# Kernel tuning notes

Measured on AMD Instinct MI355X. Metric: run time of the kernel, lower is better.

The kernel has to match this reference:

```python
import jax, jax.numpy as jnp
import numpy as np

T, D_IN, D_OUT = 8192, 1024, 1024
TRACE, CONTEXT = 64, 16


def setup_inputs() -> dict:
    key = jax.random.key(0)
    ks = jax.random.split(key, 8)
    x = jax.random.normal(ks[0], (T, D_IN), jnp.float32)
    state_re = jnp.zeros((1, TRACE, CONTEXT), jnp.float32)
    state_im = jnp.zeros((1, TRACE, CONTEXT), jnp.float32)
    start = jax.random.bernoulli(ks[1], 0.01, (T,))
    next_done = jax.random.bernoulli(ks[2], 0.01, (T,))
    lim_in = 1.0 / np.sqrt(D_IN)
    W_pre = jax.random.uniform(ks[3], (TRACE, D_IN), jnp.float32, -lim_in, lim_in)
    b_pre = jnp.zeros((TRACE,), jnp.float32)
    W_skip = jax.random.uniform(ks[4], (D_OUT, D_IN), jnp.float32, -lim_in, lim_in)
    b_skip = jnp.zeros((D_OUT,), jnp.float32)
    d_mix = 2 * TRACE * CONTEXT
    lim_mix = 1.0 / np.sqrt(d_mix)
    W_mix = jax.random.uniform(ks[5], (D_OUT, d_mix), jnp.float32, -lim_mix, lim_mix)
    b_mix = jnp.zeros((D_OUT,), jnp.float32)
    # ffa.init: deterministic decay rates a and oscillation freqs b (FFM paper)
    a = jnp.linspace(1e-6, 0.5, TRACE)
    b_freq = 2.0 * jnp.pi / jnp.linspace(1.0, 1024.0, CONTEXT)
    return dict(x=x, state_re=state_re, state_im=state_im, start=start, next_done=next_done,
                W_pre=W_pre, b_pre=b_pre, W_skip=W_skip, b_skip=b_skip,
                W_mix=W_mix, b_mix=b_mix, a=a, b_freq=b_freq)


def _ffa_scan(pre, state0, start, a, b_freq):
    """Resettable complex linear recurrence: S_t = gamma * S_{t-1} * !start_t + pre_t.
    pre: [T, m] real, state0: [1, m, c] complex. Returns [T, m, c] complex."""
    n = pre.shape[0]
    ab = (-jnp.abs(a)[:, None] + 1j * b_freq[None, :]).astype(jnp.complex64)  # [m, c]
    x_c = jnp.broadcast_to(pre[:, :, None], (n, pre.shape[1], b_freq.shape[0])).astype(jnp.complex64)
    # prepend carried-in state as an extra element with no decay (t=0) and no reset
    x_c = jnp.concatenate([state0, x_c], axis=0)
    s = jnp.concatenate([jnp.zeros((1,), bool), start.astype(bool)], axis=0)
    t = jnp.concatenate([jnp.zeros((1,), jnp.float32), jnp.ones((n,), jnp.float32)], axis=0)

    def combine(l, r):
        sl, xl, tl = l
        sr, xr, tr = r
        keep = jnp.logical_not(sr)  # right segment starts an episode -> drop left
        decay = jnp.exp(ab[None, :, :] * tr[:, None, None])  # gamma^{t_right}
        x = jnp.where(keep[:, None, None], xl * decay, jnp.zeros((), jnp.complex64)) + xr
        return (jnp.logical_or(sl, sr), x, tl * keep + tr)

    _, states, _ = jax.lax.associative_scan(combine, (s, x_c, t), axis=0)
    return states[1:]


def reference(x, state_re, state_im, start, next_done,
              W_pre, b_pre, W_skip, b_skip, W_mix, b_mix, a, b_freq):
    pre = x @ W_pre.T + b_pre                                  # [T, m]
    pre = pre / (1e-6 + jnp.linalg.norm(pre, axis=-1, keepdims=True))
    state0 = (state_re + 1j * state_im).astype(jnp.complex64)   # [1, m, c]
    states = _ffa_scan(pre, state0, start, a, b_freq)           # [T, m, c] complex
    z_in = jnp.concatenate([jnp.real(states), jnp.imag(states)], axis=-1)
    z_in = z_in.reshape(states.shape[0], -1)                    # [T, 2*m*c]
    z = z_in @ W_mix.T + b_mix                                  # [T, d_out]
    skip = x @ W_skip.T + b_skip                                # [T, d_out]
    return (z + skip, states[-1:])
```

## Files before the change

kernel.cpp:

```cpp
#include <hip/hip_runtime.h>
#include <hip/hip_bf16.h>
#include <stdint.h>

#define T_LEN 8192
#define DIN   1024
#define DOUT  1024
#define TRACE 64
#define CTX   16
#define KTOT  3072
#define CH    64
#define NCHUNK 128

#define AS1 __attribute__((address_space(1)))
#define AS3 __attribute__((address_space(3)))

using bf16 = __hip_bfloat16;
typedef __attribute__((ext_vector_type(4))) float f32x4;
typedef __attribute__((ext_vector_type(8))) short s16x8;

__device__ __forceinline__ void pack4(const float4 v, void* dst) {
    union { bf16 h[4]; uint2 u; } pk;
    pk.h[0] = __float2bfloat16(v.x); pk.h[1] = __float2bfloat16(v.y);
    pk.h[2] = __float2bfloat16(v.z); pk.h[3] = __float2bfloat16(v.w);
    *(uint2*)dst = pk.u;
}

__global__ void cvt_all(const float* __restrict__ x, const float* __restrict__ Wsk,
                        const float* __restrict__ Wmx, const float* __restrict__ Wpre,
                        bf16* __restrict__ A, bf16* __restrict__ Bc, bf16* __restrict__ Wp) {
    int idx = blockIdx.x * 256 + threadIdx.x;
    if (idx < 2097152) {
        int r = idx >> 8, c4 = (idx & 255) << 2;
        pack4(*(const float4*)(x + (size_t)r * 1024 + c4), A + (size_t)r * KTOT + c4);
    } else if (idx < 2359296) {
        int i = idx - 2097152;
        int r = i >> 8, c4 = (i & 255) << 2;
        pack4(*(const float4*)(Wsk + (size_t)r * 1024 + c4), Bc + (size_t)r * KTOT + c4);
    } else if (idx < 2883584) {
        int i = idx - 2359296;
        int r = i >> 9, c4 = (i & 511) << 2;
        pack4(*(const float4*)(Wmx + (size_t)r * 2048 + c4), Bc + (size_t)r * KTOT + 1024 + c4);
    } else if (idx < 2899968) {
        int i = idx - 2883584;
        int r = i >> 8, c4 = (i & 255) << 2;
        pack4(*(const float4*)(Wpre + (size_t)r * 1024 + c4), Wp + (size_t)r * 1024 + c4);
    }
}

__global__ __launch_bounds__(256) void pre_scan1(
    const bf16* __restrict__ A,
    const bf16* __restrict__ Wp,
    const float* __restrict__ bpre,
    const int* __restrict__ start,
    const float* __restrict__ a, const float* __restrict__ bfreq,
    float* __restrict__ pre_raw,
    float2* __restrict__ local_end,
    int* __restrict__ reset_any) {
    __shared__ short As[2][64 * 32];
    __shared__ short Bs[2][64 * 32];
    __shared__ float pn[CH][TRACE + 1];
    __shared__ float rn[CH];
    __shared__ int sf[CH];
    const int tid = threadIdx.x, lane = tid & 63, wv = tid >> 6;
    const int row0 = blockIdx.x * 64;
    const int l4 = lane >> 2, c8 = (lane & 3) * 8;

    auto stage = [&](int kt, int buf) {
        int r = wv * 16 + l4;
        const bf16* ga = A + (size_t)(row0 + r) * KTOT + kt * 32 + c8;
        const bf16* gb = Wp + (size_t)r * 1024 + kt * 32 + c8;
        __builtin_amdgcn_global_load_lds(
            (const AS1 void*)ga, (AS3 void*)&As[buf][wv * 512], 16, 0, 0);
        __builtin_amdgcn_global_load_lds(
            (const AS1 void*)gb, (AS3 void*)&Bs[buf][wv * 512], 16, 0, 0);
    };

    f32x4 acc[4];
#pragma unroll
    for (int j = 0; j < 4; ++j) acc[j] = (f32x4)0.0f;

    stage(0, 0);
    __syncthreads();
    int buf = 0;
    const int lr = lane & 15, lk = (lane >> 4) * 8;
    for (int kt = 0; kt < 32; ++kt) {
        if (kt + 1 < 32) stage(kt + 1, buf ^ 1);
        s16x8 af = *(const s16x8*)&As[buf][(wv * 16 + lr) * 32 + lk];
        s16x8 bfr[4];
#pragma unroll
        for (int j = 0; j < 4; ++j)
            bfr[j] = *(const s16x8*)&Bs[buf][(j * 16 + lr) * 32 + lk];
#pragma unroll
        for (int j = 0; j < 4; ++j)
            acc[j] = __builtin_amdgcn_mfma_f32_16x16x32_bf16(af, bfr[j], acc[j], 0, 0, 0);
        __syncthreads();
        buf ^= 1;
    }
    const int lg = lane >> 4;
#pragma unroll
    for (int j = 0; j < 4; ++j) {
        int col = j * 16 + lr;
        float bias = bpre[col];
#pragma unroll
        for (int r = 0; r < 4; ++r) {
            int rl = wv * 16 + lg * 4 + r;
            float v = acc[j][r] + bias;
            pn[rl][col] = v;
            pre_raw[(size_t)(row0 + rl) * TRACE + col] = v;
        }
    }
    if (tid < CH) sf[tid] = start[row0 + tid];
    __syncthreads();
    if (tid < CH) {
        float s = 0.f;
#pragma unroll
        for (int m = 0; m < TRACE; ++m) { float v = pn[tid][m]; s += v * v; }
        rn[tid] = 1.0f / (1e-6f + sqrtf(s));
        int any = __any(sf[tid] != 0);
        if (tid == 0) reset_any[blockIdx.x] = any;
    }
    __syncthreads();
#pragma unroll
    for (int q = 0; q < 4; ++q) {
        int pair = tid + q * 256;
        int m = pair >> 4, c = pair & 15;
        float am = a[m], th = bfreq[c];
        float e = expf(-fabsf(am));
        float sn, cs; sincosf(th, &sn, &cs);
        float gr = e * cs, gi = e * sn;
        float sre = 0.f, sim = 0.f;
        for (int r = 0; r < CH; ++r) {
            float p = pn[r][m] * rn[r];
            if (sf[r]) { sre = p; sim = 0.f; }
            else { float t = gr * sre - gi * sim + p; sim = gr * sim + gi * sre; sre = t; }
        }
        local_end[(size_t)blockIdx.x * 1024 + pair] = make_float2(sre, sim);
    }
}

__global__ void scan_phase2(const float2* __restrict__ local_end, const int* __restrict__ reset_any,
                            const float* __restrict__ state_re, const float* __restrict__ state_im,
                            const float* __restrict__ a, const float* __restrict__ bfreq,
                            float2* __restrict__ carry_in, float* __restrict__ out_tail, int tail_n) {
    const int pair = blockIdx.x * 64 + threadIdx.x;
    const int m = pair >> 4, c = pair & 15;
    float am = a[m], th = bfreq[c];
    float e = expf(-64.f * fabsf(am));
    float sn, cs; sincosf(64.f * th, &sn, &cs);
    float gr = e * cs, gi = e * sn;
    float cre = state_re[pair], cim = state_im[pair];

    float2 pf[8]; int rsv[8];
#pragma unroll
    for (int j = 0; j < 8; ++j) { pf[j] = local_end[(size_t)j * 1024 + pair]; rsv[j] = reset_any[j]; }
    for (int kb = 0; kb < NCHUNK; kb += 8) {
        float2 cur[8]; int rs[8];
#pragma unroll
        for (int j = 0; j < 8; ++j) { cur[j] = pf[j]; rs[j] = rsv[j]; }
        if (kb + 8 < NCHUNK) {
#pragma unroll
            for (int j = 0; j < 8; ++j) {
                pf[j]  = local_end[(size_t)(kb + 8 + j) * 1024 + pair];
                rsv[j] = reset_any[kb + 8 + j];
            }
        }
#pragma unroll
        for (int j = 0; j < 8; ++j) {
            carry_in[(size_t)(kb + j) * 1024 + pair] = make_float2(cre, cim);
            if (rs[j]) { cre = cur[j].x; cim = cur[j].y; }
            else {
                float t = gr * cre - gi * cim + cur[j].x;
                cim = gr * cim + gi * cre + cur[j].y;
                cre = t;
            }
        }
    }
    if (pair < tail_n)        out_tail[pair]        = cre;
    if (1024 + pair < tail_n) out_tail[1024 + pair] = cim;
}

__global__ void scan_phase3(const float* __restrict__ pre_raw, const int* __restrict__ start,
                            const float* __restrict__ a, const float* __restrict__ bfreq,
                            const float2* __restrict__ carry_in, bf16* __restrict__ A) {
    __shared__ float pn[CH][TRACE + 1];
    __shared__ float rn[CH];
    __shared__ int sf[CH];
    const int k = blockIdx.x, tid = threadIdx.x;
    for (int idx = tid; idx < CH * TRACE; idx += 256) {
        int r = idx >> 6, m = idx & 63;
        pn[r][m] = pre_raw[(size_t)(k * CH + r) * TRACE + m];
    }
    if (tid < CH) sf[tid] = start[k * CH + tid];
    __syncthreads();
    if (tid < CH) {
        float s = 0.f;
#pragma unroll
        for (int m = 0; m < TRACE; ++m) { float v = pn[tid][m]; s += v * v; }
        rn[tid] = 1.0f / (1e-6f + sqrtf(s));
    }
    __syncthreads();
#pragma unroll
    for (int q = 0; q < 2; ++q) {
        int p0 = q * 512 + tid * 2;
        int m = p0 >> 4, c0 = p0 & 15;
        float am = a[m];
        float e = expf(-fabsf(am));
        float sn0, cs0, sn1, cs1;
        sincosf(bfreq[c0], &sn0, &cs0);
        sincosf(bfreq[c0 + 1], &sn1, &cs1);
        float gr0 = e * cs0, gi0 = e * sn0;
        float gr1 = e * cs1, gi1 = e * sn1;
        float4 ci = *(const float4*)&carry_in[(size_t)k * 1024 + p0];
        float sre0 = ci.x, sim0 = ci.y, sre1 = ci.z, sim1 = ci.w;
        for (int r = 0; r < CH; ++r) {
            float p = pn[r][m] * rn[r];
            if (sf[r]) { sre0 = p; sim0 = 0.f; sre1 = p; sim1 = 0.f; }
            else {
                float t0 = gr0 * sre0 - gi0 * sim0 + p; sim0 = gr0 * sim0 + gi0 * sre0; sre0 = t0;
                float t1 = gr1 * sre1 - gi1 * sim1 + p; sim1 = gr1 * sim1 + gi1 * sre1; sre1 = t1;
            }
            size_t off = (size_t)(k * CH + r) * KTOT + 1024 + m * 32;
            union { bf16 h[2]; uint32_t u; } pr, pi;
            pr.h[0] = __float2bfloat16(sre0); pr.h[1] = __float2bfloat16(sre1);
            pi.h[0] = __float2bfloat16(sim0); pi.h[1] = __float2bfloat16(sim1);
            *(uint32_t*)(A + off + c0)      = pr.u;
            *(uint32_t*)(A + off + 16 + c0) = pi.u;
        }
    }
}

__global__ __launch_bounds__(512) void gemm_main(const bf16* __restrict__ A,
                                                 const bf16* __restrict__ B,
                                                 const float* __restrict__ bskip,
                                                 const float* __restrict__ bmix,
                                                 float* __restrict__ out) {
    __shared__ short As[3][256 * 64];
    __shared__ short Bs[3][128 * 64];
    const int tid = threadIdx.x;
    const int lane = tid & 63, wv = tid >> 6;
    const int wm = wv >> 1, wn = wv & 1;
    const int wg = blockIdx.x;
    const int xcd = wg & 7, idx = wg >> 3;
    const int row0 = (xcd * 4 + (idx >> 3)) * 256;
    const int col0 = (idx & 7) * 128;

    const int rl8 = lane >> 3;
    const int u8  = lane & 7;

    auto stage = [&](int kt, int bsel) {
#pragma unroll
        for (int j = 0; j < 4; ++j) {
            int r = wv * 32 + j * 8 + rl8;
            int ksw = (u8 ^ (r & 7)) << 3;
            const bf16* ga = A + (size_t)(row0 + r) * KTOT + kt * 64 + ksw;
            __builtin_amdgcn_global_load_lds((const AS1 void*)ga,
                (AS3 void*)&As[bsel][(wv * 32 + j * 8) * 64], 16, 0, 0);
        }
#pragma unroll
        for (int j = 0; j < 2; ++j) {
            int r = wv * 16 + j * 8 + rl8;
            int ksw = (u8 ^ (r & 7)) << 3;
            const bf16* gb = B + (size_t)(col0 + r) * KTOT + kt * 64 + ksw;
            __builtin_amdgcn_global_load_lds((const AS1 void*)gb,
                (AS3 void*)&Bs[bsel][(wv * 16 + j * 8) * 64], 16, 0, 0);
        }
    };

    f32x4 acc[4][4];
#pragma unroll
    for (int i = 0; i < 4; ++i)
#pragma unroll
        for (int j = 0; j < 4; ++j) acc[i][j] = (f32x4)0.0f;

    stage(0, 0); stage(1, 1);

    const int lr = lane & 15, hi = lane >> 4;
    int sw[2];
    sw[0] = ((hi)     ^ (lr & 7)) << 3;
    sw[1] = ((4 + hi) ^ (lr & 7)) << 3;

    const int NT = KTOT / 64;
    auto kstep = [&](int t, int bsel) __attribute__((always_inline)) {
        if (t < NT - 1) asm volatile("s_waitcnt vmcnt(6)" ::: "memory");
        else            asm volatile("s_waitcnt vmcnt(0)" ::: "memory");
        __builtin_amdgcn_s_barrier();
        if (t + 2 < NT) { int b2 = bsel + 2; if (b2 >= 3) b2 -= 3; stage(t + 2, b2); }
        s16x8 af[4][2], bfr[4][2];
#pragma unroll
        for (int kk = 0; kk < 2; ++kk) {
#pragma unroll
            for (int i = 0; i < 4; ++i)
                af[i][kk] = *(const s16x8*)&As[bsel][(wm * 64 + i * 16 + lr) * 64 + sw[kk]];
#pragma unroll
            for (int j = 0; j < 4; ++j)
                bfr[j][kk] = *(const s16x8*)&Bs[bsel][(wn * 64 + j * 16 + lr) * 64 + sw[kk]];
        }
        __builtin_amdgcn_s_setprio(1);
#pragma unroll
        for (int kk = 0; kk < 2; ++kk)
#pragma unroll
            for (int i = 0; i < 4; ++i)
#pragma unroll
                for (int j = 0; j < 4; ++j)
                    acc[i][j] = __builtin_amdgcn_mfma_f32_16x16x32_bf16(af[i][kk], bfr[j][kk], acc[i][j], 0, 0, 0);
        __builtin_amdgcn_s_setprio(0);
    };

    for (int tt = 0; tt < NT; tt += 3) {
        kstep(tt,     0);
        kstep(tt + 1, 1);
        kstep(tt + 2, 2);
    }

    const int lg = lane >> 4;
#pragma unroll
    for (int j = 0; j < 4; ++j) {
        int col = col0 + wn * 64 + j * 16 + lr;
        float bias = bskip[col] + bmix[col];
#pragma unroll
        for (int i = 0; i < 4; ++i) {
            int rbase = row0 + wm * 64 + i * 16 + lg * 4;
#pragma unroll
            for (int r = 0; r < 4; ++r)
                out[(size_t)(rbase + r) * DOUT + col] = acc[i][j][r] + bias;
        }
    }
}

extern "C" void kernel_launch(void* const* d_in, const int* in_sizes, int n_in,
                              void* d_out, int out_size, void* d_ws, size_t ws_size,
                              hipStream_t stream) {
    const float* x        = (const float*)d_in[0];
    const float* state_re = (const float*)d_in[1];
    const float* state_im = (const float*)d_in[2];
    const int*   start    = (const int*)d_in[3];
    const float* W_pre    = (const float*)d_in[5];
    const float* b_pre    = (const float*)d_in[6];
    const float* W_skip   = (const float*)d_in[7];
    const float* b_skip   = (const float*)d_in[8];
    const float* W_mix    = (const float*)d_in[9];
    const float* b_mix    = (const float*)d_in[10];
    const float* a_dec    = (const float*)d_in[11];
    const float* b_freq   = (const float*)d_in[12];

    uint8_t* ws = (uint8_t*)d_ws;
    bf16*  A         = (bf16*)(ws);
    bf16*  Bc        = (bf16*)(ws + 50331648);
    bf16*  Wp        = (bf16*)(ws + 56623104);
    float* pre_raw   = (float*)(ws + 56754176);
    float2* local_end= (float2*)(ws + 58851328);
    float2* carry_in = (float2*)(ws + 59899904);
    int*   reset_any = (int*)(ws + 60948480);

    cvt_all<<<dim3((2899968 + 255) / 256), 256, 0, stream>>>(x, W_skip, W_mix, W_pre, A, Bc, Wp);

    pre_scan1<<<dim3(NCHUNK), 256, 0, stream>>>(A, Wp, b_pre, start, a_dec, b_freq,
                                                pre_raw, local_end, reset_any);
    int tail_n = out_size - 8192 * 1024;
    if (tail_n < 0) tail_n = 0;
    if (tail_n > 2048) tail_n = 2048;
    scan_phase2<<<dim3(16), 64, 0, stream>>>(local_end, reset_any, state_re, state_im, a_dec, b_freq,
                                             carry_in, (float*)d_out + 8192 * 1024, tail_n);
    scan_phase3<<<dim3(NCHUNK), 256, 0, stream>>>(pre_raw, start, a_dec, b_freq, carry_in, A);

    gemm_main<<<dim3(256), 512, 0, stream>>>(A, Bc, b_skip, b_mix, (float*)d_out);
}
```

Before: 128.7 us.

## Split GEMM k-steps into half-phases interleaving staged loads with MFMA

Restructures the main GEMM loop so each k-tile runs as two phases, each issuing half of the next global-to-LDS prefetch, loading half the B fragments and running half the MFMAs, with a barrier after every phase. The aim is to spread memory issue across compute and overlap LDS reads with matrix work more evenly, and to hoist the swizzle computation. In exchange it doubles the number of barriers per k-tile and adds explicit lgkmcnt waits and sched barriers that may serialize work.

```diff
diff --git a/kernel.cpp b/kernel.cpp
--- a/kernel.cpp
+++ b/kernel.cpp
@@ -240,30 +240,27 @@
     const int lane = tid & 63, wv = tid >> 6;
     const int wm = wv >> 1, wn = wv & 1;
     const int wg = blockIdx.x;
-    const int xcd = wg & 7, idx = wg >> 3;
-    const int row0 = (xcd * 4 + (idx >> 3)) * 256;
-    const int col0 = (idx & 7) * 128;
+    const int xcd = wg & 7, bidx = wg >> 3;
+    const int row0 = (xcd * 4 + (bidx >> 3)) * 256;
+    const int col0 = (bidx & 7) * 128;
 
     const int rl8 = lane >> 3;
     const int u8  = lane & 7;
-
-    auto stage = [&](int kt, int bsel) {
-#pragma unroll
-        for (int j = 0; j < 4; ++j) {
+    const int ksw = (u8 ^ rl8) << 3;
+
+    auto stageBatch = [&](int su, int bd, int sb) {
+#pragma unroll
+        for (int jj = 0; jj < 2; ++jj) {
+            int j = sb * 2 + jj;
             int r = wv * 32 + j * 8 + rl8;
-            int ksw = (u8 ^ (r & 7)) << 3;
-            const bf16* ga = A + (size_t)(row0 + r) * KTOT + kt * 64 + ksw;
+            const bf16* ga = A + (size_t)(row0 + r) * KTOT + su * 64 + ksw;
             __builtin_amdgcn_global_load_lds((const AS1 void*)ga,
-                (AS3 void*)&As[bsel][(wv * 32 + j * 8) * 64], 16, 0, 0);
-        }
-#pragma unroll
-        for (int j = 0; j < 2; ++j) {
-            int r = wv * 16 + j * 8 + rl8;
-            int ksw = (u8 ^ (r & 7)) << 3;
-            const bf16* gb = B + (size_t)(col0 + r) * KTOT + kt * 64 + ksw;
-            __builtin_amdgcn_global_load_lds((const AS1 void*)gb,
-                (AS3 void*)&Bs[bsel][(wv * 16 + j * 8) * 64], 16, 0, 0);
-        }
+                (AS3 void*)&As[bd][(wv * 32 + j * 8) * 64], 16, 0, 0);
+        }
+        int rb = wv * 16 + sb * 8 + rl8;
+        const bf16* gb = B + (size_t)(col0 + rb) * KTOT + su * 64 + ksw;
+        __builtin_amdgcn_global_load_lds((const AS1 void*)gb,
+            (AS3 void*)&Bs[bd][(wv * 16 + sb * 8) * 64], 16, 0, 0);
     };
 
     f32x4 acc[4][4];
@@ -272,45 +269,70 @@
 #pragma unroll
         for (int j = 0; j < 4; ++j) acc[i][j] = (f32x4)0.0f;
 
-    stage(0, 0); stage(1, 1);
-
     const int lr = lane & 15, hi = lane >> 4;
-    int sw[2];
-    sw[0] = ((hi)     ^ (lr & 7)) << 3;
-    sw[1] = ((4 + hi) ^ (lr & 7)) << 3;
-
-    const int NT = KTOT / 64;
-    auto kstep = [&](int t, int bsel) __attribute__((always_inline)) {
-        if (t < NT - 1) asm volatile("s_waitcnt vmcnt(6)" ::: "memory");
-        else            asm volatile("s_waitcnt vmcnt(0)" ::: "memory");
+    const int sw0 = ((0 + hi) ^ (lr & 7)) << 3;
+    const int sw1 = ((4 + hi) ^ (lr & 7)) << 3;
+
+    s16x8 af[4][2], bfr[4][2];
+
+    auto phase = [&](int b, int h, int su, int bd, int sb, int vm) {
+        if (su >= 0) stageBatch(su, bd, sb);
+        if (h == 0) {
+#pragma unroll
+            for (int i = 0; i < 4; ++i) {
+                af[i][0] = *(const s16x8*)&As[b][(wm * 64 + i * 16 + lr) * 64 + sw0];
+                af[i][1] = *(const s16x8*)&As[b][(wm * 64 + i * 16 + lr) * 64 + sw1];
+            }
+#pragma unroll
+            for (int j = 0; j < 2; ++j) {
+                bfr[j][0] = *(const s16x8*)&Bs[b][(wn * 64 + j * 16 + lr) * 64 + sw0];
+                bfr[j][1] = *(const s16x8*)&Bs[b][(wn * 64 + j * 16 + lr) * 64 + sw1];
+            }
+        } else {
+#pragma unroll
+            for (int j = 2; j < 4; ++j) {
+                bfr[j][0] = *(const s16x8*)&Bs[b][(wn * 64 + j * 16 + lr) * 64 + sw0];
+                bfr[j][1] = *(const s16x8*)&Bs[b][(wn * 64 + j * 16 + lr) * 64 + sw1];
+            }
+        }
+        asm volatile("s_waitcnt lgkmcnt(0)" ::: "memory");
+        __builtin_amdgcn_sched_barrier(0);
+        __builtin_amdgcn_s_setprio(1);
+#pragma unroll
+        for (int kk = 0; kk < 2; ++kk)
+#pragma unroll
+            for (int i = 0; i < 4; ++i)
+#pragma unroll
+                for (int jj = 0; jj < 2; ++jj) {
+                    int j = h * 2 + jj;
+                    acc[i][j] = __builtin_amdgcn_mfma_f32_16x16x32_bf16(af[i][kk], bfr[j][kk], acc[i][j], 0, 0, 0);
+                }
+        __builtin_amdgcn_s_setprio(0);
+        if (vm == 6)      asm volatile("s_waitcnt vmcnt(6)" ::: "memory");
+        else if (vm == 0) asm volatile("s_waitcnt vmcnt(0)" ::: "memory");
         __builtin_amdgcn_s_barrier();
-        if (t + 2 < NT) { int b2 = bsel + 2; if (b2 >= 3) b2 -= 3; stage(t + 2, b2); }
-        s16x8 af[4][2], bfr[4][2];
-#pragma unroll
-        for (int kk = 0; kk < 2; ++kk) {
-#pragma unroll
-            for (int i = 0; i < 4; ++i)
-                af[i][kk] = *(const s16x8*)&As[bsel][(wm * 64 + i * 16 + lr) * 64 + sw[kk]];
-#pragma unroll
-            for (int j = 0; j < 4; ++j)
-                bfr[j][kk] = *(const s16x8*)&Bs[bsel][(wn * 64 + j * 16 + lr) * 64 + sw[kk]];
-        }
-        __builtin_amdgcn_s_setprio(1);
-#pragma unroll
-        for (int kk = 0; kk < 2; ++kk)
-#pragma unroll
-            for (int i = 0; i < 4; ++i)
-#pragma unroll
-                for (int j = 0; j < 4; ++j)
-                    acc[i][j] = __builtin_amdgcn_mfma_f32_16x16x32_bf16(af[i][kk], bfr[j][kk], acc[i][j], 0, 0, 0);
-        __builtin_amdgcn_s_setprio(0);
     };
 
-    for (int tt = 0; tt < NT; tt += 3) {
-        kstep(tt,     0);
-        kstep(tt + 1, 1);
-        kstep(tt + 2, 2);
-    }
+    stageBatch(0, 0, 0); stageBatch(0, 0, 1);
+    stageBatch(1, 1, 0); stageBatch(1, 1, 1);
+    asm volatile("s_waitcnt vmcnt(6)" ::: "memory");
+    __builtin_amdgcn_s_barrier();
+
+    for (int t = 0; t < 15; ++t) {
+        int u2 = 3 * t + 2;
+        phase(0, 0, u2,     2, 0, -1);
+        phase(0, 1, u2,     2, 1,  6);
+        phase(1, 0, u2 + 1, 0, 0, -1);
+        phase(1, 1, u2 + 1, 0, 1,  6);
+        phase(2, 0, u2 + 2, 1, 0, -1);
+        phase(2, 1, u2 + 2, 1, 1,  6);
+    }
+    phase(0, 0, 47, 2, 0, -1);
+    phase(0, 1, 47, 2, 1,  6);
+    phase(1, 0, -1, 0, 0, -1);
+    phase(1, 1, -1, 0, 0,  0);
+    phase(2, 0, -1, 0, 0, -1);
+    phase(2, 1, -1, 0, 0, -1);
 
     const int lg = lane >> 4;
 #pragma unroll
```

Result: slower. 131.7 us (+2.4%).
